# Performance work log

Hardware: AMD Instinct MI355X
Metric: run time of the kernel (lower is better)

## Reference

```python
import jax, jax.numpy as jnp
import numpy as np

KS = 17  # structuring element size
R = KS // 2  # radius 8


def _ellipse_kernel():
    # replicates cv2.getStructuringElement(cv2.MORPH_ELLIPSE, (17, 17)):
    # per row dy, fill columns within dx = round(sqrt(r^2 - dy^2))
    k = np.zeros((KS, KS), np.float32)
    for i in range(KS):
        dy = i - R
        dx = int(round(np.sqrt(max(0.0, float(R * R - dy * dy)))))
        k[i, R - dx:R + dx + 1] = 1.0
    return k


def _morph(v, kern, erode):
    # exact TF min-plus erosion2d / max-plus dilation2d with SAME padding
    # (pad +inf for erosion, -inf for dilation), filters = kern per channel.
    B, H, W, C = v.shape
    pad_val = np.inf if erode else -np.inf
    sgn = -1.0 if erode else 1.0
    red = jnp.min if erode else jnp.max
    comb = jnp.minimum if erode else jnp.maximum
    vp = jnp.pad(v, ((0, 0), (0, 0), (R, R), (0, 0)), constant_values=pad_val)
    X = jnp.stack([vp[:, :, k:k + W, :] for k in range(KS)], axis=0)
    # per kernel row dy: 1D min/max-plus correlation along x
    rows = [red(X + sgn * kern[dy][:, None, None, None, None], axis=0) for dy in range(KS)]
    Rst = jnp.pad(jnp.stack(rows, axis=0), ((0, 0), (0, 0), (R, R), (0, 0), (0, 0)), constant_values=pad_val)
    out = Rst[0][:, 0:H]
    for dy in range(1, KS):
        out = comb(out, Rst[dy][:, dy:dy + H])
    return out


def _mask_edges(masks, kern):
    # flip border rows/cols (corners flipped twice -> original)
    m = jnp.concatenate([1.0 - masks[:, :1], masks[:, 1:-1], 1.0 - masks[:, -1:]], axis=1)
    m = jnp.concatenate([1.0 - m[:, :, :1], m[:, :, 1:-1], 1.0 - m[:, :, -1:]], axis=2)
    eroded = _morph(m, kern, erode=True) + 1.0
    dilated = _morph(m, kern, erode=False) - 1.0
    return dilated - eroded


def setup_inputs() -> dict:
    key = jax.random.key(0)
    k1, k2, k3 = jax.random.split(key, 3)
    B, H, W, C = 8, 512, 512, 3
    in_detections = jax.random.randint(k1, (B, H, W, C), 0, 2).astype(jnp.float32)
    p_detections = jax.random.normal(k2, (B, H, W, C), dtype=jnp.float32)
    edge_weight = 1.0 + 39.0 * jax.random.uniform(k3, (1, 1, 1, C), dtype=jnp.float32)
    in_masks = jnp.ones((B, C), dtype=jnp.float32)
    logvars = -3.0 * jnp.ones((1, C), dtype=jnp.float32)
    return {"in_masks": in_masks, "in_detections": in_detections,
            "p_detections": p_detections, "edge_weight": edge_weight,
            "logvars": logvars}


def reference(in_masks, in_detections, p_detections, edge_weight, logvars):
    kern = jnp.asarray(_ellipse_kernel())
    edges = _mask_edges(in_detections, kern)  # (B,H,W,C)
    weights = 1.0 + (edge_weight - 1.0) * edges
    weights = weights / jnp.sum(weights, axis=(1, 2), keepdims=True)
    pix = jnp.where(in_detections == 1.0,
                    jnp.maximum(0.0, 1.0 - p_detections) ** 2,
                    jnp.maximum(0.0, p_detections) ** 2)
    raw = jnp.sum(weights * pix, axis=(1, 2))  # (B,C)
    losses = jnp.exp(-logvars) * raw + logvars  # (B,C)
    return jnp.mean(in_masks * losses, axis=1)  # (B,)
```

## Files before the change

kernel.cpp:

```cpp
#include <hip/hip_runtime.h>
#include <stdint.h>


#define TILE 16
#define ROWS 32
#define NT   32
#define PLS  90
#define MAGICV 0x7F3B9E1Du

__global__ __launch_bounds__(1024) void k_fused(const float* __restrict__ det,
                                                const float* __restrict__ pdet,
                                                float* partials,
                                                unsigned int* tags,
                                                const float* __restrict__ in_masks,
                                                const float* __restrict__ ew,
                                                const float* __restrict__ lv,
                                                float* __restrict__ out) {
  __shared__ uint64_t mb[3][ROWS][9];
  __shared__ uint64_t pl[ROWS][PLS];
  __shared__ uint64_t eg[3][TILE][8];
  __shared__ float red[16][6];
  __shared__ int cw[3][2];
  __shared__ float term[8][3];

  int blk = blockIdx.x;
  int b = blk & 7;
  int tile = blk >> 3;
  int r0 = tile * TILE;
  int tid = threadIdx.x;
  int wv = tid >> 6, lane = tid & 63;

  for (int it = 0; it < 16; ++it) {
    int task = wv * 16 + it;
    int rl = task >> 3, w = task & 7;
    int grow = r0 - 8 + rl;
    uint64_t b0 = 0, b1 = 0, b2 = 0;
    if (grow >= 0 && grow < 512) {
      size_t base = (((((size_t)b << 9) + grow) << 9) + (w << 6) + lane) * 3;
      float d0 = det[base], d1 = det[base + 1], d2 = det[base + 2];
      b0 = __ballot(d0 == 1.0f);
      b1 = __ballot(d1 == 1.0f);
      b2 = __ballot(d2 == 1.0f);
    }
    if (lane == 0) { mb[0][rl][w] = b0; mb[1][rl][w] = b1; mb[2][rl][w] = b2; }
  }
  __syncthreads();

  const int PD[9] = {5, 5, 5, 4, 4, 3, 2, 1, 0};

  for (int ch = 0; ch < 3; ++ch) {
    if (tid < 512) {
      int side = tid >> 8;
      int t2 = tid & 255;
      int rl = t2 >> 3, w = t2 & 7;
      int grow = r0 - 8 + rl;
      bool valid = (grow >= 0 && grow < 512);
      uint64_t x = 0, xl = 0, xh = 0;
      if (valid) {
        x = mb[ch][rl][w];
        xl = (w > 0) ? mb[ch][rl][w - 1] : 0;
        xh = (w < 7) ? mb[ch][rl][w + 1] : 0;
        if (grow == 0 || grow == 511) {
          x = ~x;
          xl = (w > 0) ? ~xl : 0;
          xh = (w < 7) ? ~xh : 0;
        }
        if (w == 0) x ^= 1ull;
        if (w == 7) x ^= (1ull << 63);
        if (side) {
          x = ~x;
          xl = (w > 0) ? ~xl : 0;
          xh = (w < 7) ? ~xh : 0;
        }
      }
      uint64_t* P = pl[rl];
      if (!side) P[w] = x;
      uint64_t d = x;
#pragma unroll
      for (int s = 1; s <= 8; ++s) {
        d |= (x << s) | (xl >> (64 - s)) | (x >> s) | (xh << (64 - s));
        if (s >= 4) P[(s - 3 + side * 5) * 8 + w] = d;
      }
    }
    __syncthreads();

    if (tid < 128) {
      int rl = tid >> 3, w = tid & 7;
      uint64_t dil = 0, erc = 0;
#pragma unroll
      for (int dy = -8; dy <= 8; ++dy) {
        int ady = dy < 0 ? -dy : dy;
        int pr = rl + 8 + dy;
        if (ady == 8) {
          int grow = r0 - 8 + pr;
          uint64_t m = pl[pr][w];
          dil |= m;
          erc |= (grow >= 0 && grow < 512) ? ~m : 0;
        } else {
          dil |= pl[pr][PD[ady] * 8 + w];
          erc |= pl[pr][(PD[ady] + 5) * 8 + w];
        }
      }
      uint64_t e = dil & erc;
      eg[ch][rl][w] = e;
      int c = __popcll(e);
#pragma unroll
      for (int off = 32; off >= 1; off >>= 1) c += __shfl_xor(c, off);
      if (lane == 0) cw[ch][wv] = c;
    }
    __syncthreads();
  }

  float sA0 = 0, sA1 = 0, sA2 = 0, sE0 = 0, sE1 = 0, sE2 = 0;
#pragma unroll
  for (int it = 0; it < 8; ++it) {
    int task = wv * 8 + it;
    int rl = task >> 3, w = task & 7;
    int grow = r0 + rl;
    size_t base = (((((size_t)b << 9) + grow) << 9) + (w << 6) + lane) * 3;
    float p0 = pdet[base], p1 = pdet[base + 1], p2 = pdet[base + 2];
    uint64_t D0 = mb[0][rl + 8][w], D1 = mb[1][rl + 8][w], D2 = mb[2][rl + 8][w];
    uint64_t E0 = eg[0][rl][w], E1 = eg[1][rl][w], E2 = eg[2][rl][w];
    float v0 = ((D0 >> lane) & 1) ? 1.0f - p0 : p0; v0 = fmaxf(v0, 0.f); v0 *= v0;
    float v1 = ((D1 >> lane) & 1) ? 1.0f - p1 : p1; v1 = fmaxf(v1, 0.f); v1 *= v1;
    float v2 = ((D2 >> lane) & 1) ? 1.0f - p2 : p2; v2 = fmaxf(v2, 0.f); v2 *= v2;
    sA0 += v0; sA1 += v1; sA2 += v2;
    if ((E0 >> lane) & 1) sE0 += v0;
    if ((E1 >> lane) & 1) sE1 += v1;
    if ((E2 >> lane) & 1) sE2 += v2;
  }
#pragma unroll
  for (int off = 32; off >= 1; off >>= 1) {
    sA0 += __shfl_xor(sA0, off); sA1 += __shfl_xor(sA1, off); sA2 += __shfl_xor(sA2, off);
    sE0 += __shfl_xor(sE0, off); sE1 += __shfl_xor(sE1, off); sE2 += __shfl_xor(sE2, off);
  }
  if (lane == 0) {
    red[wv][0] = sA0; red[wv][1] = sA1; red[wv][2] = sA2;
    red[wv][3] = sE0; red[wv][4] = sE1; red[wv][5] = sE2;
  }
  __syncthreads();

  if (tid < 6) {
    float s = 0.f;
    for (int i = 0; i < 16; ++i) s += red[i][tid];
    __hip_atomic_store(&partials[blk * 9 + tid], s,
                       __ATOMIC_RELAXED, __HIP_MEMORY_SCOPE_AGENT);
  } else if (tid < 9) {
    int chx = tid - 6;
    __hip_atomic_store(&partials[blk * 9 + tid], (float)(cw[chx][0] + cw[chx][1]),
                       __ATOMIC_RELAXED, __HIP_MEMORY_SCOPE_AGENT);
  }
  __syncthreads();
  if (tid == 0) {
    __hip_atomic_store(&tags[blk], MAGICV,
                       __ATOMIC_RELEASE, __HIP_MEMORY_SCOPE_AGENT);
  }

  if (blk != 0) return;
  if (tid < 256) {
    while (__hip_atomic_load(&tags[tid], __ATOMIC_ACQUIRE,
                             __HIP_MEMORY_SCOPE_AGENT) != MAGICV) {
      __builtin_amdgcn_s_sleep(8);
    }
  }
  __syncthreads();

  if (tid < 24) {
    int b8 = tid / 3, ch = tid - 3 * b8;
    float sA = 0.f, sE = 0.f, cn = 0.f;
    for (int t = 0; t < NT; ++t) {
      float* P = partials + (size_t)((t << 3) | b8) * 9;
      sA += __hip_atomic_load(&P[ch], __ATOMIC_RELAXED, __HIP_MEMORY_SCOPE_AGENT);
      sE += __hip_atomic_load(&P[3 + ch], __ATOMIC_RELAXED, __HIP_MEMORY_SCOPE_AGENT);
      cn += __hip_atomic_load(&P[6 + ch], __ATOMIC_RELAXED, __HIP_MEMORY_SCOPE_AGENT);
    }
    float w1 = ew[ch] - 1.0f;
    float S = 262144.0f + w1 * cn;
    float raw = (sA + w1 * sE) / S;
    term[b8][ch] = in_masks[b8 * 3 + ch] * (expf(-lv[ch]) * raw + lv[ch]);
  }
  __syncthreads();
  if (tid < 8) out[tid] = (term[tid][0] + term[tid][1] + term[tid][2]) * (1.0f / 3.0f);
}

extern "C" void kernel_launch(void* const* d_in, const int* in_sizes, int n_in,
                              void* d_out, int out_size, void* d_ws, size_t ws_size,
                              hipStream_t stream) {
  const float* in_masks = (const float*)d_in[0];
  const float* det = (const float*)d_in[1];
  const float* pdet = (const float*)d_in[2];
  const float* ew = (const float*)d_in[3];
  const float* lv = (const float*)d_in[4];
  float* out = (float*)d_out;

  float* partials = (float*)d_ws;
  unsigned int* tags = (unsigned int*)(partials + 256 * 9);

  k_fused<<<256, 1024, 0, stream>>>(det, pdet, partials, tags,
                                    in_masks, ew, lv, out);
}
```

Measured before the change: 24.03 us.

## Share halo mask bits between neighbor blocks via global bitmasks and flags

Each block now reads only its own 16 rows of det, packs them into bitmasks, and publishes them to a global workspace. It then spin-waits on flags from the vertically adjacent tiles and loads their halo bits, instead of re-reading 8 halo rows of float det on each side. pdet loads are hoisted to the start so they overlap the det loads and the synchronisation. This roughly halves det traffic, at the cost of inter-block spin waits that assume all 256 blocks are co-resident, and higher register use from holding pv and dv.

```diff
diff --git a/kernel.cpp b/kernel.cpp
--- a/kernel.cpp
+++ b/kernel.cpp
@@ -6,12 +6,13 @@
 #define ROWS 32
 #define NT   32
 #define PLS  90
-#define MAGICV 0x7F3B9E1Du
+#define MAGIC64 0x7F3B9E1DC0FFEE42ull
 
 __global__ __launch_bounds__(1024) void k_fused(const float* __restrict__ det,
                                                 const float* __restrict__ pdet,
+                                                uint64_t* dbits,
                                                 float* partials,
-                                                unsigned int* tags,
+                                                unsigned long long* tags,
                                                 const float* __restrict__ in_masks,
                                                 const float* __restrict__ ew,
                                                 const float* __restrict__ lv,
@@ -30,19 +31,78 @@
   int tid = threadIdx.x;
   int wv = tid >> 6, lane = tid & 63;
 
-  for (int it = 0; it < 16; ++it) {
-    int task = wv * 16 + it;
-    int rl = task >> 3, w = task & 7;
-    int grow = r0 - 8 + rl;
-    uint64_t b0 = 0, b1 = 0, b2 = 0;
-    if (grow >= 0 && grow < 512) {
-      size_t base = (((((size_t)b << 9) + grow) << 9) + (w << 6) + lane) * 3;
-      float d0 = det[base], d1 = det[base + 1], d2 = det[base + 2];
-      b0 = __ballot(d0 == 1.0f);
-      b1 = __ballot(d1 == 1.0f);
-      b2 = __ballot(d2 == 1.0f);
-    }
-    if (lane == 0) { mb[0][rl][w] = b0; mb[1][rl][w] = b1; mb[2][rl][w] = b2; }
+  float pv[8][3];
+#pragma unroll
+  for (int it = 0; it < 8; ++it) {
+    int task = wv * 8 + it;
+    int rl = task >> 3, w = task & 7;
+    size_t base = (((((size_t)b << 9) + (r0 + rl)) << 9) + (w << 6) + lane) * 3;
+    pv[it][0] = pdet[base];
+    pv[it][1] = pdet[base + 1];
+    pv[it][2] = pdet[base + 2];
+  }
+
+  float dv[8][3];
+#pragma unroll
+  for (int it = 0; it < 8; ++it) {
+    int task = wv * 8 + it;
+    int rl = task >> 3, w = task & 7;
+    size_t base = (((((size_t)b << 9) + (r0 + rl)) << 9) + (w << 6) + lane) * 3;
+    dv[it][0] = det[base];
+    dv[it][1] = det[base + 1];
+    dv[it][2] = det[base + 2];
+  }
+#pragma unroll
+  for (int it = 0; it < 8; ++it) {
+    int task = wv * 8 + it;
+    int rl = task >> 3, w = task & 7;
+    uint64_t b0 = __ballot(dv[it][0] == 1.0f);
+    uint64_t b1 = __ballot(dv[it][1] == 1.0f);
+    uint64_t b2 = __ballot(dv[it][2] == 1.0f);
+    if (lane == 0) {
+      mb[0][rl + 8][w] = b0;
+      mb[1][rl + 8][w] = b1;
+      mb[2][rl + 8][w] = b2;
+      size_t o = ((size_t)(r0 + rl) << 3) + w;
+      __hip_atomic_store(&dbits[(((size_t)(b * 3 + 0)) << 12) + o], b0,
+                         __ATOMIC_RELAXED, __HIP_MEMORY_SCOPE_AGENT);
+      __hip_atomic_store(&dbits[(((size_t)(b * 3 + 1)) << 12) + o], b1,
+                         __ATOMIC_RELAXED, __HIP_MEMORY_SCOPE_AGENT);
+      __hip_atomic_store(&dbits[(((size_t)(b * 3 + 2)) << 12) + o], b2,
+                         __ATOMIC_RELAXED, __HIP_MEMORY_SCOPE_AGENT);
+    }
+  }
+  __syncthreads();
+  if (tid == 0)
+    __hip_atomic_store(&tags[blk], MAGIC64,
+                       __ATOMIC_RELEASE, __HIP_MEMORY_SCOPE_AGENT);
+
+  if (tid == 0 && tile > 0) {
+    while (__hip_atomic_load(&tags[blk - 8], __ATOMIC_ACQUIRE,
+                             __HIP_MEMORY_SCOPE_AGENT) != MAGIC64)
+      __builtin_amdgcn_s_sleep(2);
+  }
+  if (tid == 64 && tile < NT - 1) {
+    while (__hip_atomic_load(&tags[blk + 8], __ATOMIC_ACQUIRE,
+                             __HIP_MEMORY_SCOPE_AGENT) != MAGIC64)
+      __builtin_amdgcn_s_sleep(2);
+  }
+  __syncthreads();
+
+  if (tid < 384) {
+    int ch = tid >> 7;
+    int rem = tid & 127;
+    int side = rem >> 6;
+    int idx = rem & 63;
+    int rh = idx >> 3, w = idx & 7;
+    int grow = side == 0 ? (r0 - 8 + rh) : (r0 + TILE + rh);
+    int rlds = side == 0 ? rh : (24 + rh);
+    uint64_t v = 0;
+    if (grow >= 0 && grow < 512)
+      v = __hip_atomic_load(&dbits[(((size_t)(b * 3 + ch)) << 12) +
+                                   ((size_t)grow << 3) + w],
+                            __ATOMIC_RELAXED, __HIP_MEMORY_SCOPE_AGENT);
+    mb[ch][rlds][w] = v;
   }
   __syncthreads();
 
@@ -116,9 +176,7 @@
   for (int it = 0; it < 8; ++it) {
     int task = wv * 8 + it;
     int rl = task >> 3, w = task & 7;
-    int grow = r0 + rl;
-    size_t base = (((((size_t)b << 9) + grow) << 9) + (w << 6) + lane) * 3;
-    float p0 = pdet[base], p1 = pdet[base + 1], p2 = pdet[base + 2];
+    float p0 = pv[it][0], p1 = pv[it][1], p2 = pv[it][2];
     uint64_t D0 = mb[0][rl + 8][w], D1 = mb[1][rl + 8][w], D2 = mb[2][rl + 8][w];
     uint64_t E0 = eg[0][rl][w], E1 = eg[1][rl][w], E2 = eg[2][rl][w];
     float v0 = ((D0 >> lane) & 1) ? 1.0f - p0 : p0; v0 = fmaxf(v0, 0.f); v0 *= v0;
@@ -151,17 +209,15 @@
                        __ATOMIC_RELAXED, __HIP_MEMORY_SCOPE_AGENT);
   }
   __syncthreads();
-  if (tid == 0) {
-    __hip_atomic_store(&tags[blk], MAGICV,
+  if (tid == 0)
+    __hip_atomic_store(&tags[256 + blk], MAGIC64,
                        __ATOMIC_RELEASE, __HIP_MEMORY_SCOPE_AGENT);
-  }
 
   if (blk != 0) return;
   if (tid < 256) {
-    while (__hip_atomic_load(&tags[tid], __ATOMIC_ACQUIRE,
-                             __HIP_MEMORY_SCOPE_AGENT) != MAGICV) {
+    while (__hip_atomic_load(&tags[256 + tid], __ATOMIC_ACQUIRE,
+                             __HIP_MEMORY_SCOPE_AGENT) != MAGIC64)
       __builtin_amdgcn_s_sleep(8);
-    }
   }
   __syncthreads();
 
@@ -193,9 +249,11 @@
   const float* lv = (const float*)d_in[4];
   float* out = (float*)d_out;
 
-  float* partials = (float*)d_ws;
-  unsigned int* tags = (unsigned int*)(partials + 256 * 9);
-
-  k_fused<<<256, 1024, 0, stream>>>(det, pdet, partials, tags,
+  uint64_t* dbits = (uint64_t*)d_ws;
+  float* partials = (float*)(dbits + (size_t)24 * 512 * 8);
+  unsigned long long* tags =
+      (unsigned long long*)(partials + 256 * 9);
+
+  k_fused<<<256, 1024, 0, stream>>>(det, pdet, dbits, partials, tags,
                                     in_masks, ew, lv, out);
 }
```

Result: slower. 28.60 us (+19.1%).
